# Kernel optimization log

Measured on AMD Instinct MI355X. Metric: run time of the kernel, lower is better.

The kernel has to match this reference:

```python
import jax, jax.numpy as jnp
import numpy as np

H = 1024      # hidden_size
NH = 16       # num_heads
HD = H // NH  # head_dim
BETA = 1.0
STEPS = 2
EPS_NORM = 1e-12  # F.normalize eps
EPS_LN = 1e-5     # LayerNorm eps


def setup_inputs() -> dict:
    key = jax.random.key(0)
    ks = jax.random.split(key, 10)
    s = 1.0 / np.sqrt(H)
    return {
        "hidden_states": jax.random.normal(ks[0], (2, 2048, H), jnp.float32),
        "Wq": jax.random.normal(ks[1], (H, H), jnp.float32) * s,
        "bq": jnp.zeros((H,), jnp.float32),
        "Wk": jax.random.normal(ks[2], (H, H), jnp.float32) * s,
        "bk": jnp.zeros((H,), jnp.float32),
        "Wv": jax.random.normal(ks[3], (H, H), jnp.float32) * s,
        "bv": jnp.zeros((H,), jnp.float32),
        "Wo": jax.random.normal(ks[4], (H, H), jnp.float32) * s,
        "bo": jnp.zeros((H,), jnp.float32),
        "ln_w": jnp.ones((H,), jnp.float32),
        "ln_b": jnp.zeros((H,), jnp.float32),
    }


def _l2norm(x):
    n = jnp.linalg.norm(x, axis=-1, keepdims=True)
    return x / jnp.maximum(n, EPS_NORM)


def reference(hidden_states, Wq, bq, Wk, bk, Wv, bv, Wo, bo, ln_w, ln_b):
    B, S, _ = hidden_states.shape
    residual = hidden_states
    # LayerNorm
    mu = jnp.mean(hidden_states, axis=-1, keepdims=True)
    var = jnp.mean(jnp.square(hidden_states - mu), axis=-1, keepdims=True)
    x = (hidden_states - mu) * jax.lax.rsqrt(var + EPS_LN) * ln_w + ln_b
    # projections -> [B,S,NH,HD]
    q = (x @ Wq + bq).reshape(B, S, NH, HD)
    k = (x @ Wk + bk).reshape(B, S, NH, HD)
    v = (x @ Wv + bv).reshape(B, S, NH, HD)
    # cosine-normalized Hopfield retrieval (normalization only once, before loop)
    q = _l2norm(q)
    k = _l2norm(k)
    state = q
    for _ in range(STEPS):
        sim = jnp.einsum('bqhd,bkhd->bqhk', state, k)
        att = jax.nn.softmax(BETA * sim, axis=-1)
        state = jnp.einsum('bqhk,bkhd->bqhd', att, v)
    o = state.reshape(B, S, H) @ Wo + bo
    return residual + o
```

## Files before the change

kernel.cpp:

```cpp
#include <hip/hip_runtime.h>
#include <hip/hip_bf16.h>
#include <math.h>

#define HDIM 1024
#define NHEADS 16
#define HEADD 64
#define SEQLEN 2048
#define NBATCH 2
#define NROWS (NBATCH*SEQLEN)
#define NBH (NBATCH*NHEADS)
#define LOG2E 1.44269504f
#define NT 32

typedef float f32x4 __attribute__((ext_vector_type(4)));
typedef float f32x16 __attribute__((ext_vector_type(16)));
typedef short short8 __attribute__((ext_vector_type(8)));
typedef unsigned short us4v __attribute__((ext_vector_type(4)));

#define GLOBAL_AS __attribute__((address_space(1)))
#define LDS_AS __attribute__((address_space(3)))

union F4 { float4 v; float f[4]; };
union PW { unsigned int u[4]; short8 s; };

static __device__ __forceinline__ unsigned short f2bf(float x) {
    __hip_bfloat16 h = __float2bfloat16(x);
    return *(unsigned short*)&h;
}

__global__ __launch_bounds__(256) void ln_kernel(
        const float* __restrict__ x, const float* __restrict__ w,
        const float* __restrict__ b, unsigned short* __restrict__ xn) {
    int row = blockIdx.x;
    F4 vv; vv.v = ((const float4*)(x + (size_t)row*HDIM))[threadIdx.x];
    float s  = vv.f[0]+vv.f[1]+vv.f[2]+vv.f[3];
    float ss = vv.f[0]*vv.f[0]+vv.f[1]*vv.f[1]+vv.f[2]*vv.f[2]+vv.f[3]*vv.f[3];
    #pragma unroll
    for (int off = 32; off > 0; off >>= 1) {
        s  += __shfl_xor(s, off);
        ss += __shfl_xor(ss, off);
    }
    __shared__ float red[8];
    int wid = threadIdx.x >> 6;
    if ((threadIdx.x & 63) == 0) { red[wid] = s; red[wid+4] = ss; }
    __syncthreads();
    s  = red[0]+red[1]+red[2]+red[3];
    ss = red[4]+red[5]+red[6]+red[7];
    float mean = s * (1.0f/HDIM);
    float var  = ss * (1.0f/HDIM) - mean*mean;
    float rstd = rsqrtf(var + 1e-5f);
    F4 wv; wv.v = ((const float4*)w)[threadIdx.x];
    F4 bv; bv.v = ((const float4*)b)[threadIdx.x];
    us4v o;
    #pragma unroll
    for (int j = 0; j < 4; ++j)
        o[j] = f2bf((vv.f[j]-mean)*rstd*wv.f[j] + bv.f[j]);
    *(us4v*)(xn + (size_t)row*HDIM + threadIdx.x*4) = o;
}

__global__ __launch_bounds__(256) void wconv_kernel(
        const float* __restrict__ W0, const float* __restrict__ W1,
        const float* __restrict__ W2, const float* __restrict__ W3,
        unsigned short* __restrict__ WtBase) {
    __shared__ unsigned short T[64*72];
    int z = blockIdx.z;
    const float* W = (z == 0) ? W0 : (z == 1) ? W1 : (z == 2) ? W2 : W3;
    unsigned short* Wt = WtBase + (size_t)z*HDIM*HDIM;
    int k0 = blockIdx.x*64, n0 = blockIdx.y*64;
    int t = threadIdx.x;
    #pragma unroll
    for (int it = 0; it < 4; ++it) {
        int r = (t>>4) + it*16;
        int c = (t&15)*4;
        F4 x; x.v = *(const float4*)(W + (size_t)(k0+r)*HDIM + n0 + c);
        #pragma unroll
        for (int j = 0; j < 4; ++j) T[(c+j)*72 + r] = f2bf(x.f[j]);
    }
    __syncthreads();
    #pragma unroll
    for (int it = 0; it < 2; ++it) {
        int n = (t>>3) + it*32;
        int ch = t&7;
        short8 rowv = *(const short8*)(T + n*72 + ch*8);
        *(short8*)(Wt + (size_t)(n0+n)*HDIM + k0 + ch*8) = rowv;
    }
}

__global__ __launch_bounds__(256) void gemm_qkv_kernel(
        const unsigned short* __restrict__ A,
        const unsigned short* __restrict__ WtBase,
        const float* __restrict__ bq, const float* __restrict__ bk,
        const float* __restrict__ bv,
        unsigned short* __restrict__ qb, unsigned short* __restrict__ kb,
        unsigned short* __restrict__ vt) {
    __shared__ unsigned short As[2][128*64];
    __shared__ unsigned short Bs[2][128*64];
    int m0 = blockIdx.x * 128;
    int yy = blockIdx.y;
    int mat = yy >> 3;
    int n0 = (yy & 7) * 128;
    const unsigned short* Wt = WtBase + (size_t)mat*HDIM*HDIM;
    const float* bias = (mat == 0) ? bq : (mat == 1) ? bk : bv;
    int t = threadIdx.x;
    int wid = t >> 6, l = t & 63;
    int wm = wid >> 1, wn = wid & 1;
    int lq = l & 15, g = l >> 4;
    f32x4 acc[4][4];
    #pragma unroll
    for (int mi = 0; mi < 4; ++mi)
        #pragma unroll
        for (int ni = 0; ni < 4; ++ni) acc[mi][ni] = 0.0f;

    auto STAGE = [&](int b, int k0) {
        #pragma unroll
        for (int i = 0; i < 4; ++i) {
            int idx = t + 256*i;
            int r = idx >> 3, ch = idx & 7;
            int gch = ch ^ (r & 7);
            __builtin_amdgcn_global_load_lds(
                (const GLOBAL_AS void*)(A + (size_t)(m0+r)*HDIM + k0 + gch*8),
                (LDS_AS void*)((char*)&As[b][0] + idx*16), 16, 0, 0);
            __builtin_amdgcn_global_load_lds(
                (const GLOBAL_AS void*)(Wt + (size_t)(n0+r)*HDIM + k0 + gch*8),
                (LDS_AS void*)((char*)&Bs[b][0] + idx*16), 16, 0, 0);
        }
    };

    STAGE(0, 0);
    asm volatile("s_waitcnt vmcnt(0)" ::: "memory");
    __builtin_amdgcn_s_barrier();
    asm volatile("" ::: "memory");
    int buf = 0;
    for (int ks = 0; ks < 16; ++ks) {
        if (ks < 15) STAGE(buf^1, (ks+1)*64);
        const char* Ab = (const char*)&As[buf][0];
        const char* Bb = (const char*)&Bs[buf][0];
        #pragma unroll
        for (int kc = 0; kc < 2; ++kc) {
            short8 af[4], bf[4];
            #pragma unroll
            for (int mi = 0; mi < 4; ++mi) {
                int r = wm*64 + mi*16 + lq;
                af[mi] = *(const short8*)(Ab + r*128 + (((kc*4+g) ^ (r&7))<<4));
            }
            #pragma unroll
            for (int ni = 0; ni < 4; ++ni) {
                int r = wn*64 + ni*16 + lq;
                bf[ni] = *(const short8*)(Bb + r*128 + (((kc*4+g) ^ (r&7))<<4));
            }
            #pragma unroll
            for (int mi = 0; mi < 4; ++mi)
                #pragma unroll
                for (int ni = 0; ni < 4; ++ni)
                    acc[mi][ni] = __builtin_amdgcn_mfma_f32_16x16x32_bf16(
                        af[mi], bf[ni], acc[mi][ni], 0, 0, 0);
        }
        asm volatile("s_waitcnt vmcnt(0)" ::: "memory");
        __builtin_amdgcn_s_barrier();
        asm volatile("" ::: "memory");
        buf ^= 1;
    }
    float bvv[4];
    #pragma unroll
    for (int ni = 0; ni < 4; ++ni) bvv[ni] = bias[n0 + wn*64 + ni*16 + lq];
    #pragma unroll
    for (int mi = 0; mi < 4; ++mi)
        #pragma unroll
        for (int ni = 0; ni < 4; ++ni)
            #pragma unroll
            for (int i = 0; i < 4; ++i) acc[mi][ni][i] += bvv[ni];
    int h = (n0 >> 6) + wn;
    if (mat <= 1) {
        unsigned short* outp = (mat == 0) ? qb : kb;
        float oscale = (mat == 0) ? LOG2E : 1.0f;
        #pragma unroll
        for (int mi = 0; mi < 4; ++mi) {
            f32x4 ss = 0.0f;
            #pragma unroll
            for (int ni = 0; ni < 4; ++ni)
                #pragma unroll
                for (int i = 0; i < 4; ++i) ss[i] += acc[mi][ni][i]*acc[mi][ni][i];
            #pragma unroll
            for (int off = 1; off < 16; off <<= 1)
                #pragma unroll
                for (int i = 0; i < 4; ++i) ss[i] += __shfl_xor(ss[i], off);
            #pragma unroll
            for (int i = 0; i < 4; ++i) {
                float sc = oscale / fmaxf(sqrtf(ss[i]), 1e-12f);
                int m = m0 + wm*64 + mi*16 + g*4 + i;
                int bb = m >> 11, sq = m & (SEQLEN-1);
                unsigned short* orow = outp
                    + ((size_t)(bb*NHEADS + h)*SEQLEN + sq)*HEADD;
                #pragma unroll
                for (int ni = 0; ni < 4; ++ni)
                    orow[ni*16 + lq] = f2bf(acc[mi][ni][i] * sc);
            }
        }
    } else {
        #pragma unroll
        for (int mi = 0; mi < 4; ++mi) {
            int m = m0 + wm*64 + mi*16 + g*4;
            int bb = m >> 11, sq = m & (SEQLEN-1);
            #pragma unroll
            for (int ni = 0; ni < 4; ++ni) {
                int d = ni*16 + lq;
                us4v pk;
                #pragma unroll
                for (int i = 0; i < 4; ++i) pk[i] = f2bf(acc[mi][ni][i]);
                *(us4v*)(vt + ((size_t)(bb*NHEADS + h)*HEADD + d)*SEQLEN + sq) = pk;
            }
        }
    }
}

__global__ __launch_bounds__(256) void gemm_o_kernel(
        const unsigned short* __restrict__ A,
        const unsigned short* __restrict__ Wt,
        const float* __restrict__ bias,
        const float* __restrict__ residual,
        float* __restrict__ out) {
    __shared__ unsigned short As[2][128*64];
    __shared__ unsigned short Bs[2][64*64];
    int m0 = blockIdx.x * 128;
    int n0 = blockIdx.y * 64;
    int t = threadIdx.x;
    int wid = t >> 6, l = t & 63;
    int wm = wid >> 1, wn = wid & 1;
    int lq = l & 15, g = l >> 4;
    f32x4 acc[4][2];
    #pragma unroll
    for (int mi = 0; mi < 4; ++mi)
        #pragma unroll
        for (int ni = 0; ni < 2; ++ni) acc[mi][ni] = 0.0f;

    auto STAGE = [&](int b, int k0) {
        #pragma unroll
        for (int i = 0; i < 4; ++i) {
            int idx = t + 256*i;
            int r = idx >> 3, ch = idx & 7;
            int gch = ch ^ (r & 7);
            __builtin_amdgcn_global_load_lds(
                (const GLOBAL_AS void*)(A + (size_t)(m0+r)*HDIM + k0 + gch*8),
                (LDS_AS void*)((char*)&As[b][0] + idx*16), 16, 0, 0);
        }
        #pragma unroll
        for (int i = 0; i < 2; ++i) {
            int idx = t + 256*i;
            int r = idx >> 3, ch = idx & 7;
            int gch = ch ^ (r & 7);
            __builtin_amdgcn_global_load_lds(
                (const GLOBAL_AS void*)(Wt + (size_t)(n0+r)*HDIM + k0 + gch*8),
                (LDS_AS void*)((char*)&Bs[b][0] + idx*16), 16, 0, 0);
        }
    };

    STAGE(0, 0);
    asm volatile("s_waitcnt vmcnt(0)" ::: "memory");
    __builtin_amdgcn_s_barrier();
    asm volatile("" ::: "memory");
    int buf = 0;
    for (int ks = 0; ks < 16; ++ks) {
        if (ks < 15) STAGE(buf^1, (ks+1)*64);
        const char* Ab = (const char*)&As[buf][0];
        const char* Bb = (const char*)&Bs[buf][0];
        #pragma unroll
        for (int kc = 0; kc < 2; ++kc) {
            short8 af[4], bf[2];
            #pragma unroll
            for (int mi = 0; mi < 4; ++mi) {
                int r = wm*64 + mi*16 + lq;
                af[mi] = *(const short8*)(Ab + r*128 + (((kc*4+g) ^ (r&7))<<4));
            }
            #pragma unroll
            for (int ni = 0; ni < 2; ++ni) {
                int r = wn*32 + ni*16 + lq;
                bf[ni] = *(const short8*)(Bb + r*128 + (((kc*4+g) ^ (r&7))<<4));
            }
            #pragma unroll
            for (int mi = 0; mi < 4; ++mi)
                #pragma unroll
                for (int ni = 0; ni < 2; ++ni)
                    acc[mi][ni] = __builtin_amdgcn_mfma_f32_16x16x32_bf16(
                        af[mi], bf[ni], acc[mi][ni], 0, 0, 0);
        }
        asm volatile("s_waitcnt vmcnt(0)" ::: "memory");
        __builtin_amdgcn_s_barrier();
        asm volatile("" ::: "memory");
        buf ^= 1;
    }
    float bvv[2];
    #pragma unroll
    for (int ni = 0; ni < 2; ++ni) bvv[ni] = bias[n0 + wn*32 + ni*16 + lq];
    #pragma unroll
    for (int mi = 0; mi < 4; ++mi)
        #pragma unroll
        for (int i = 0; i < 4; ++i) {
            int m = m0 + wm*64 + mi*16 + g*4 + i;
            float* orow = out + (size_t)m*HDIM;
            const float* rrow = residual + (size_t)m*HDIM;
            #pragma unroll
            for (int ni = 0; ni < 2; ++ni) {
                int n = n0 + wn*32 + ni*16 + lq;
                orow[n] = acc[mi][ni][i] + bvv[ni] + rrow[n];
            }
        }
}

__global__ __launch_bounds__(512, 4) void attn_fused_kernel(
        const unsigned short* __restrict__ qg, const unsigned short* __restrict__ kg,
        const unsigned short* __restrict__ vtg, unsigned short* __restrict__ outp) {
    __shared__ char L[4*16384];
    int b = blockIdx.x;
    int bh = (b & 7)*4 + ((b >> 3) & 3);
    int q0 = (b >> 5) * 128;
    int t = threadIdx.x;
    int wid = t >> 6, l = t & 63;
    int wq = wid >> 1, ks = wid & 1;
    int q = l & 31, hi = l >> 5, r7 = q & 7;
    short8 qf[4];
    {
        const unsigned short* qrow = qg + ((size_t)bh*SEQLEN + q0 + wq*32 + q)*HEADD;
        #pragma unroll
        for (int dc = 0; dc < 4; ++dc) qf[dc] = *(const short8*)(qrow + dc*16 + hi*8);
    }
    int koffK0 = q*128 + (((0 + hi) ^ r7) << 4) + ks*4096;
    int koffK1 = q*128 + (((2 + hi) ^ r7) << 4) + ks*4096;
    int koffK2 = q*128 + (((4 + hi) ^ r7) << 4) + ks*4096;
    int koffK3 = q*128 + (((6 + hi) ^ r7) << 4) + ks*4096;
    int vofA = q*128 + (((4*ks + hi) ^ r7) << 4);
    int vofB = q*128 + (((4*ks + 2 + hi) ^ r7) << 4);

    f32x16 o0 = 0.0f, o1 = 0.0f;
    float ls = 0.0f;
    const unsigned short* Kg = kg + (size_t)bh*SEQLEN*HEADD;
    const unsigned short* Vg = vtg + (size_t)bh*HEADD*SEQLEN;
    unsigned int* slot = (unsigned int*)(L + wq*4096);
    float* slsum = (float*)(L + 16384 + wq*256);

    int sr = t >> 3, sch = t & 7;
    int sgch = sch ^ (sr & 7);
    const unsigned short* Ksrc = Kg + sr*HEADD + sgch*8;
    const unsigned short* Vsrc = Vg + (size_t)sr*SEQLEN + sgch*8;
    auto STAGE = [&](int buf, int kt) {
        __builtin_amdgcn_global_load_lds(
            (const GLOBAL_AS void*)(Ksrc + (size_t)kt*4096),
            (LDS_AS void*)(L + buf*16384 + t*16), 16, 0, 0);
        __builtin_amdgcn_global_load_lds(
            (const GLOBAL_AS void*)(Vsrc + kt*64),
            (LDS_AS void*)(L + buf*16384 + 8192 + t*16), 16, 0, 0);
    };

    auto doPair = [&](const char* A, const char* B) {
        short8 ka0 = *(const short8*)(A + koffK0);
        short8 ka1 = *(const short8*)(A + koffK1);
        short8 ka2 = *(const short8*)(A + koffK2);
        short8 ka3 = *(const short8*)(A + koffK3);
        f32x16 sA = 0.0f;
        sA = __builtin_amdgcn_mfma_f32_32x32x16_bf16(ka0, qf[0], sA, 0, 0, 0);
        sA = __builtin_amdgcn_mfma_f32_32x32x16_bf16(ka1, qf[1], sA, 0, 0, 0);
        sA = __builtin_amdgcn_mfma_f32_32x32x16_bf16(ka2, qf[2], sA, 0, 0, 0);
        sA = __builtin_amdgcn_mfma_f32_32x32x16_bf16(ka3, qf[3], sA, 0, 0, 0);
        __builtin_amdgcn_sched_barrier(0);
        short8 kb0 = *(const short8*)(B + koffK0);
        short8 kb1 = *(const short8*)(B + koffK1);
        short8 kb2 = *(const short8*)(B + koffK2);
        short8 kb3 = *(const short8*)(B + koffK3);
        f32x16 sB = 0.0f;
        sB = __builtin_amdgcn_mfma_f32_32x32x16_bf16(kb0, qf[0], sB, 0, 0, 0);
        sB = __builtin_amdgcn_mfma_f32_32x32x16_bf16(kb1, qf[1], sB, 0, 0, 0);
        sB = __builtin_amdgcn_mfma_f32_32x32x16_bf16(kb2, qf[2], sB, 0, 0, 0);
        sB = __builtin_amdgcn_mfma_f32_32x32x16_bf16(kb3, qf[3], sB, 0, 0, 0);
        __builtin_amdgcn_sched_barrier(0);
        unsigned int wA[8];
        float pA = 0.0f;
        #pragma unroll
        for (int i = 0; i < 8; ++i) {
            float e0 = __builtin_amdgcn_exp2f(sA[2*i]);
            float e1 = __builtin_amdgcn_exp2f(sA[2*i+1]);
            pA += e0 + e1;
            asm("v_cvt_pk_bf16_f32 %0, %1, %2" : "=v"(wA[i]) : "v"(e0), "v"(e1));
        }
        asm volatile("v_permlane32_swap_b32 %0, %1" : "+v"(wA[0]), "+v"(wA[2]));
        asm volatile("v_permlane32_swap_b32 %0, %1" : "+v"(wA[1]), "+v"(wA[3]));
        asm volatile("v_permlane32_swap_b32 %0, %1" : "+v"(wA[4]), "+v"(wA[6]));
        asm volatile("v_permlane32_swap_b32 %0, %1" : "+v"(wA[5]), "+v"(wA[7]));
        __builtin_amdgcn_sched_barrier(0);
        unsigned int wB[8];
        float pB = 0.0f;
        #pragma unroll
        for (int i = 0; i < 8; ++i) {
            float e0 = __builtin_amdgcn_exp2f(sB[2*i]);
            float e1 = __builtin_amdgcn_exp2f(sB[2*i+1]);
            pB += e0 + e1;
            asm("v_cvt_pk_bf16_f32 %0, %1, %2" : "=v"(wB[i]) : "v"(e0), "v"(e1));
        }
        ls += pA + pB;
        asm volatile("v_permlane32_swap_b32 %0, %1" : "+v"(wB[0]), "+v"(wB[2]));
        asm volatile("v_permlane32_swap_b32 %0, %1" : "+v"(wB[1]), "+v"(wB[3]));
        asm volatile("v_permlane32_swap_b32 %0, %1" : "+v"(wB[4]), "+v"(wB[6]));
        asm volatile("v_permlane32_swap_b32 %0, %1" : "+v"(wB[5]), "+v"(wB[7]));
        __builtin_amdgcn_sched_barrier(0);
        {
            PW pa, pb;
            pa.u[0]=wA[0]; pa.u[1]=wA[1]; pa.u[2]=wA[2]; pa.u[3]=wA[3];
            pb.u[0]=wA[4]; pb.u[1]=wA[5]; pb.u[2]=wA[6]; pb.u[3]=wA[7];
            short8 va0 = *(const short8*)(A + 8192 + vofA);
            short8 va1 = *(const short8*)(A + 8192 + vofA + 4096);
            short8 vb0 = *(const short8*)(A + 8192 + vofB);
            short8 vb1 = *(const short8*)(A + 8192 + vofB + 4096);
            __builtin_amdgcn_s_setprio(1);
            o0 = __builtin_amdgcn_mfma_f32_32x32x16_bf16(va0, pa.s, o0, 0, 0, 0);
            o1 = __builtin_amdgcn_mfma_f32_32x32x16_bf16(va1, pa.s, o1, 0, 0, 0);
            o0 = __builtin_amdgcn_mfma_f32_32x32x16_bf16(vb0, pb.s, o0, 0, 0, 0);
            o1 = __builtin_amdgcn_mfma_f32_32x32x16_bf16(vb1, pb.s, o1, 0, 0, 0);
            __builtin_amdgcn_s_setprio(0);
        }
        __builtin_amdgcn_sched_barrier(0);
        {
            PW pa, pb;
            pa.u[0]=wB[0]; pa.u[1]=wB[1]; pa.u[2]=wB[2]; pa.u[3]=wB[3];
            pb.u[0]=wB[4]; pb.u[1]=wB[5]; pb.u[2]=wB[6]; pb.u[3]=wB[7];
            short8 va0 = *(const short8*)(B + 8192 + vofA);
            short8 va1 = *(const short8*)(B + 8192 + vofA + 4096);
            short8 vb0 = *(const short8*)(B + 8192 + vofB);
            short8 vb1 = *(const short8*)(B + 8192 + vofB + 4096);
            __builtin_amdgcn_s_setprio(1);
            o0 = __builtin_amdgcn_mfma_f32_32x32x16_bf16(va0, pa.s, o0, 0, 0, 0);
            o1 = __builtin_amdgcn_mfma_f32_32x32x16_bf16(va1, pa.s, o1, 0, 0, 0);
            o0 = __builtin_amdgcn_mfma_f32_32x32x16_bf16(vb0, pb.s, o0, 0, 0, 0);
            o1 = __builtin_amdgcn_mfma_f32_32x32x16_bf16(vb1, pb.s, o1, 0, 0, 0);
            __builtin_amdgcn_s_setprio(0);
        }
    };

    auto runPass = [&]() {
        #pragma unroll 1
        for (int p = 0; p < NT/2; ++p) {
            int ba = (p & 1) * 2;
            if (p < NT/2 - 1) { STAGE(ba^2, 2*p+2); STAGE((ba^2)+1, 2*p+3); }
            doPair(L + ba*16384, L + (ba+1)*16384);
            asm volatile("s_waitcnt vmcnt(0)" ::: "memory");
            __builtin_amdgcn_s_barrier();
            asm volatile("" ::: "memory");
        }
    };

    STAGE(0, 0); STAGE(1, 1);
    asm volatile("s_waitcnt vmcnt(0)" ::: "memory");
    __builtin_amdgcn_s_barrier();
    asm volatile("" ::: "memory");
    runPass();
    ls += __shfl_xor(ls, 32);
    if (ks == 1) {
        #pragma unroll
        for (int i = 0; i < 8; ++i) {
            unsigned int u;
            asm("v_cvt_pk_bf16_f32 %0, %1, %2" : "=v"(u) : "v"(o0[2*i]), "v"(o0[2*i+1]));
            slot[i*64 + l] = u;
            asm("v_cvt_pk_bf16_f32 %0, %1, %2" : "=v"(u) : "v"(o1[2*i]), "v"(o1[2*i+1]));
            slot[(8+i)*64 + l] = u;
        }
        slsum[l] = ls;
        asm volatile("s_waitcnt lgkmcnt(0)" ::: "memory");
    }
    __builtin_amdgcn_s_barrier();
    asm volatile("" ::: "memory");
    if (ks == 0) {
        #pragma unroll
        for (int i = 0; i < 8; ++i) {
            unsigned int u = slot[i*64 + l];
            o0[2*i]   += __uint_as_float(u << 16);
            o0[2*i+1] += __uint_as_float(u & 0xffff0000u);
            u = slot[(8+i)*64 + l];
            o1[2*i]   += __uint_as_float(u << 16);
            o1[2*i+1] += __uint_as_float(u & 0xffff0000u);
        }
        float osc = LOG2E / (ls + slsum[l]);
        unsigned int w0[8], w1[8];
        #pragma unroll
        for (int i = 0; i < 8; ++i) {
            float a0 = o0[2*i]*osc, a1 = o0[2*i+1]*osc;
            asm("v_cvt_pk_bf16_f32 %0, %1, %2" : "=v"(w0[i]) : "v"(a0), "v"(a1));
            float b0 = o1[2*i]*osc, b1 = o1[2*i+1]*osc;
            asm("v_cvt_pk_bf16_f32 %0, %1, %2" : "=v"(w1[i]) : "v"(b0), "v"(b1));
        }
        asm volatile("v_permlane32_swap_b32 %0, %1" : "+v"(w0[0]), "+v"(w0[2]));
        asm volatile("v_permlane32_swap_b32 %0, %1" : "+v"(w0[1]), "+v"(w0[3]));
        asm volatile("v_permlane32_swap_b32 %0, %1" : "+v"(w0[4]), "+v"(w0[6]));
        asm volatile("v_permlane32_swap_b32 %0, %1" : "+v"(w0[5]), "+v"(w0[7]));
        asm volatile("v_permlane32_swap_b32 %0, %1" : "+v"(w1[0]), "+v"(w1[2]));
        asm volatile("v_permlane32_swap_b32 %0, %1" : "+v"(w1[1]), "+v"(w1[3]));
        asm volatile("v_permlane32_swap_b32 %0, %1" : "+v"(w1[4]), "+v"(w1[6]));
        asm volatile("v_permlane32_swap_b32 %0, %1" : "+v"(w1[5]), "+v"(w1[7]));
        PW pa;
        pa.u[0]=w0[0]; pa.u[1]=w0[1]; pa.u[2]=w0[2]; pa.u[3]=w0[3]; qf[0]=pa.s;
        pa.u[0]=w0[4]; pa.u[1]=w0[5]; pa.u[2]=w0[6]; pa.u[3]=w0[7]; qf[1]=pa.s;
        pa.u[0]=w1[0]; pa.u[1]=w1[1]; pa.u[2]=w1[2]; pa.u[3]=w1[3]; qf[2]=pa.s;
        pa.u[0]=w1[4]; pa.u[1]=w1[5]; pa.u[2]=w1[6]; pa.u[3]=w1[7]; qf[3]=pa.s;
        #pragma unroll
        for (int i = 0; i < 8; ++i) {
            slot[i*64 + l] = w0[i];
            slot[(8+i)*64 + l] = w1[i];
        }
        asm volatile("s_waitcnt lgkmcnt(0)" ::: "memory");
    }
    __builtin_amdgcn_s_barrier();
    asm volatile("" ::: "memory");
    if (ks == 1) {
        PW pa;
        pa.u[0]=slot[0*64+l]; pa.u[1]=slot[1*64+l]; pa.u[2]=slot[2*64+l]; pa.u[3]=slot[3*64+l]; qf[0]=pa.s;
        pa.u[0]=slot[4*64+l]; pa.u[1]=slot[5*64+l]; pa.u[2]=slot[6*64+l]; pa.u[3]=slot[7*64+l]; qf[1]=pa.s;
        pa.u[0]=slot[8*64+l]; pa.u[1]=slot[9*64+l]; pa.u[2]=slot[10*64+l]; pa.u[3]=slot[11*64+l]; qf[2]=pa.s;
        pa.u[0]=slot[12*64+l]; pa.u[1]=slot[13*64+l]; pa.u[2]=slot[14*64+l]; pa.u[3]=slot[15*64+l]; qf[3]=pa.s;
    }
    asm volatile("s_waitcnt lgkmcnt(0)" ::: "memory");
    __builtin_amdgcn_s_barrier();
    asm volatile("" ::: "memory");
    o0 = 0.0f; o1 = 0.0f; ls = 0.0f;
    STAGE(0, 0); STAGE(1, 1);
    asm volatile("s_waitcnt vmcnt(0)" ::: "memory");
    __builtin_amdgcn_s_barrier();
    asm volatile("" ::: "memory");
    runPass();
    ls += __shfl_xor(ls, 32);
    if (ks == 1) {
        #pragma unroll
        for (int i = 0; i < 8; ++i) {
            unsigned int u;
            asm("v_cvt_pk_bf16_f32 %0, %1, %2" : "=v"(u) : "v"(o0[2*i]), "v"(o0[2*i+1]));
            slot[i*64 + l] = u;
            asm("v_cvt_pk_bf16_f32 %0, %1, %2" : "=v"(u) : "v"(o1[2*i]), "v"(o1[2*i+1]));
            slot[(8+i)*64 + l] = u;
        }
        slsum[l] = ls;
        asm volatile("s_waitcnt lgkmcnt(0)" ::: "memory");
    }
    __builtin_amdgcn_s_barrier();
    asm volatile("" ::: "memory");
    if (ks == 0) {
        #pragma unroll
        for (int i = 0; i < 8; ++i) {
            unsigned int u = slot[i*64 + l];
            o0[2*i]   += __uint_as_float(u << 16);
            o0[2*i+1] += __uint_as_float(u & 0xffff0000u);
            u = slot[(8+i)*64 + l];
            o1[2*i]   += __uint_as_float(u << 16);
            o1[2*i+1] += __uint_as_float(u & 0xffff0000u);
        }
        float osc = 1.0f / (ls + slsum[l]);
        int bb = bh >> 4, hh = bh & 15;
        unsigned short* orow = outp + ((size_t)bb*SEQLEN + q0 + wq*32 + q)*HDIM + hh*HEADD;
        const int dtab[8] = {0,2,8,10,16,18,24,26};
        #pragma unroll
        for (int i = 0; i < 8; ++i) {
            int d = dtab[i] + 4*hi;
            unsigned int wv;
            float a0 = o0[2*i]*osc, a1 = o0[2*i+1]*osc;
            asm("v_cvt_pk_bf16_f32 %0, %1, %2" : "=v"(wv) : "v"(a0), "v"(a1));
            *(unsigned int*)(orow + d) = wv;
            float c0 = o1[2*i]*osc, c1 = o1[2*i+1]*osc;
            asm("v_cvt_pk_bf16_f32 %0, %1, %2" : "=v"(wv) : "v"(c0), "v"(c1));
            *(unsigned int*)(orow + 32 + d) = wv;
        }
    }
}

extern "C" void kernel_launch(void* const* d_in, const int* in_sizes, int n_in,
                              void* d_out, int out_size, void* d_ws, size_t ws_size,
                              hipStream_t stream) {
    const float* hs = (const float*)d_in[0];
    const float* Wq = (const float*)d_in[1];
    const float* bq = (const float*)d_in[2];
    const float* Wk = (const float*)d_in[3];
    const float* bk = (const float*)d_in[4];
    const float* Wv = (const float*)d_in[5];
    const float* bv = (const float*)d_in[6];
    const float* Wo = (const float*)d_in[7];
    const float* bo = (const float*)d_in[8];
    const float* lw = (const float*)d_in[9];
    const float* lb = (const float*)d_in[10];
    unsigned short* ws16 = (unsigned short*)d_ws;
    const size_t NE = (size_t)NROWS * HDIM;
    const size_t WE = (size_t)HDIM * HDIM;
    unsigned short* xn  = ws16;
    unsigned short* Wtq = xn + NE;
    unsigned short* Wto = Wtq + 3*WE;
    unsigned short* qb  = Wtq + 4*WE;
    unsigned short* kb  = qb + NE;
    unsigned short* vt  = kb + NE;
    unsigned short* s2  = vt + NE;

    ln_kernel<<<NROWS, 256, 0, stream>>>(hs, lw, lb, xn);
    wconv_kernel<<<dim3(HDIM/64, HDIM/64, 4), 256, 0, stream>>>(Wq, Wk, Wv, Wo, Wtq);
    gemm_qkv_kernel<<<dim3(NROWS/128, 24), 256, 0, stream>>>(xn, Wtq, bq, bk, bv, qb, kb, vt);
    attn_fused_kernel<<<NBH*16, 512, 0, stream>>>(qb, kb, vt, s2);
    gemm_o_kernel<<<dim3(NROWS/128, HDIM/64), 256, 0, stream>>>(s2, Wto, bo, hs, (float*)d_out);
}
```

Baseline: 163.2 us.

## Double queries per attention block to reuse each K/V tile twice

Each wave now handles two 32-row query groups (A and B) against every staged K/V tile, so a block covers 256 queries and the grid halves. K and V fragments loaded from LDS are shared by both groups, which halves global K/V traffic and LDS reads per query. In exchange, register pressure doubles for accumulators and Q fragments, occupancy drops (launch bounds go from 4 to 2), and there are half as many blocks (256) to spread across the CUs.

```diff
diff --git a/kernel.cpp b/kernel.cpp
--- a/kernel.cpp
+++ b/kernel.cpp
@@ -306,22 +306,26 @@
         }
 }
 
-__global__ __launch_bounds__(512, 4) void attn_fused_kernel(
+__global__ __launch_bounds__(512, 2) void attn_fused_kernel(
         const unsigned short* __restrict__ qg, const unsigned short* __restrict__ kg,
         const unsigned short* __restrict__ vtg, unsigned short* __restrict__ outp) {
     __shared__ char L[4*16384];
     int b = blockIdx.x;
     int bh = (b & 7)*4 + ((b >> 3) & 3);
-    int q0 = (b >> 5) * 128;
+    int q0 = (b >> 5) * 256;
     int t = threadIdx.x;
     int wid = t >> 6, l = t & 63;
     int wq = wid >> 1, ks = wid & 1;
     int q = l & 31, hi = l >> 5, r7 = q & 7;
-    short8 qf[4];
+    short8 qfA[4], qfB[4];
     {
-        const unsigned short* qrow = qg + ((size_t)bh*SEQLEN + q0 + wq*32 + q)*HEADD;
-        #pragma unroll
-        for (int dc = 0; dc < 4; ++dc) qf[dc] = *(const short8*)(qrow + dc*16 + hi*8);
+        const unsigned short* qrowA = qg + ((size_t)bh*SEQLEN + q0 + wq*64 + q)*HEADD;
+        const unsigned short* qrowB = qrowA + 32*HEADD;
+        #pragma unroll
+        for (int dc = 0; dc < 4; ++dc) {
+            qfA[dc] = *(const short8*)(qrowA + dc*16 + hi*8);
+            qfB[dc] = *(const short8*)(qrowB + dc*16 + hi*8);
+        }
     }
     int koffK0 = q*128 + (((0 + hi) ^ r7) << 4) + ks*4096;
     int koffK1 = q*128 + (((2 + hi) ^ r7) << 4) + ks*4096;
@@ -330,12 +334,14 @@
     int vofA = q*128 + (((4*ks + hi) ^ r7) << 4);
     int vofB = q*128 + (((4*ks + 2 + hi) ^ r7) << 4);
 
-    f32x16 o0 = 0.0f, o1 = 0.0f;
-    float ls = 0.0f;
+    f32x16 oA0 = 0.0f, oA1 = 0.0f, oB0 = 0.0f, oB1 = 0.0f;
+    float lsA = 0.0f, lsB = 0.0f;
     const unsigned short* Kg = kg + (size_t)bh*SEQLEN*HEADD;
     const unsigned short* Vg = vtg + (size_t)bh*HEADD*SEQLEN;
-    unsigned int* slot = (unsigned int*)(L + wq*4096);
-    float* slsum = (float*)(L + 16384 + wq*256);
+    unsigned int* slotA = (unsigned int*)(L + wq*4096);
+    unsigned int* slotB = (unsigned int*)(L + 16384 + wq*4096);
+    float* slsA = (float*)(L + 32768 + wq*512);
+    float* slsB = slsA + 64;
 
     int sr = t >> 3, sch = t & 7;
     int sgch = sch ^ (sr & 7);
@@ -350,26 +356,22 @@
             (LDS_AS void*)(L + buf*16384 + 8192 + t*16), 16, 0, 0);
     };
 
-    auto doPair = [&](const char* A, const char* B) {
-        short8 ka0 = *(const short8*)(A + koffK0);
-        short8 ka1 = *(const short8*)(A + koffK1);
-        short8 ka2 = *(const short8*)(A + koffK2);
-        short8 ka3 = *(const short8*)(A + koffK3);
+    auto doTile = [&](const char* T) {
+        short8 k0 = *(const short8*)(T + koffK0);
+        short8 k1 = *(const short8*)(T + koffK1);
+        short8 k2 = *(const short8*)(T + koffK2);
+        short8 k3 = *(const short8*)(T + koffK3);
         f32x16 sA = 0.0f;
-        sA = __builtin_amdgcn_mfma_f32_32x32x16_bf16(ka0, qf[0], sA, 0, 0, 0);
-        sA = __builtin_amdgcn_mfma_f32_32x32x16_bf16(ka1, qf[1], sA, 0, 0, 0);
-        sA = __builtin_amdgcn_mfma_f32_32x32x16_bf16(ka2, qf[2], sA, 0, 0, 0);
-        sA = __builtin_amdgcn_mfma_f32_32x32x16_bf16(ka3, qf[3], sA, 0, 0, 0);
+        sA = __builtin_amdgcn_mfma_f32_32x32x16_bf16(k0, qfA[0], sA, 0, 0, 0);
+        sA = __builtin_amdgcn_mfma_f32_32x32x16_bf16(k1, qfA[1], sA, 0, 0, 0);
+        sA = __builtin_amdgcn_mfma_f32_32x32x16_bf16(k2, qfA[2], sA, 0, 0, 0);
+        sA = __builtin_amdgcn_mfma_f32_32x32x16_bf16(k3, qfA[3], sA, 0, 0, 0);
         __builtin_amdgcn_sched_barrier(0);
-        short8 kb0 = *(const short8*)(B + koffK0);
-        short8 kb1 = *(const short8*)(B + koffK1);
-        short8 kb2 = *(const short8*)(B + koffK2);
-        short8 kb3 = *(const short8*)(B + koffK3);
         f32x16 sB = 0.0f;
-        sB = __builtin_amdgcn_mfma_f32_32x32x16_bf16(kb0, qf[0], sB, 0, 0, 0);
-        sB = __builtin_amdgcn_mfma_f32_32x32x16_bf16(kb1, qf[1], sB, 0, 0, 0);
-        sB = __builtin_amdgcn_mfma_f32_32x32x16_bf16(kb2, qf[2], sB, 0, 0, 0);
-        sB = __builtin_amdgcn_mfma_f32_32x32x16_bf16(kb3, qf[3], sB, 0, 0, 0);
+        sB = __builtin_amdgcn_mfma_f32_32x32x16_bf16(k0, qfB[0], sB, 0, 0, 0);
+        sB = __builtin_amdgcn_mfma_f32_32x32x16_bf16(k1, qfB[1], sB, 0, 0, 0);
+        sB = __builtin_amdgcn_mfma_f32_32x32x16_bf16(k2, qfB[2], sB, 0, 0, 0);
+        sB = __builtin_amdgcn_mfma_f32_32x32x16_bf16(k3, qfB[3], sB, 0, 0, 0);
         __builtin_amdgcn_sched_barrier(0);
         unsigned int wA[8];
         float pA = 0.0f;
@@ -380,10 +382,16 @@
             pA += e0 + e1;
             asm("v_cvt_pk_bf16_f32 %0, %1, %2" : "=v"(wA[i]) : "v"(e0), "v"(e1));
         }
-        asm volatile("v_permlane32_swap_b32 %0, %1" : "+v"(wA[0]), "+v"(wA[2]));
-        asm volatile("v_permlane32_swap_b32 %0, %1" : "+v"(wA[1]), "+v"(wA[3]));
-        asm volatile("v_permlane32_swap_b32 %0, %1" : "+v"(wA[4]), "+v"(wA[6]));
-        asm volatile("v_permlane32_swap_b32 %0, %1" : "+v"(wA[5]), "+v"(wA[7]));
+        lsA += pA;
+        asm("v_permlane32_swap_b32 %0, %1" : "+v"(wA[0]), "+v"(wA[2]));
+        asm("v_permlane32_swap_b32 %0, %1" : "+v"(wA[1]), "+v"(wA[3]));
+        asm("v_permlane32_swap_b32 %0, %1" : "+v"(wA[4]), "+v"(wA[6]));
+        asm("v_permlane32_swap_b32 %0, %1" : "+v"(wA[5]), "+v"(wA[7]));
+        __builtin_amdgcn_sched_barrier(0);
+        short8 va0 = *(const short8*)(T + 8192 + vofA);
+        short8 va1 = *(const short8*)(T + 8192 + vofA + 4096);
+        short8 vb0 = *(const short8*)(T + 8192 + vofB);
+        short8 vb1 = *(const short8*)(T + 8192 + vofB + 4096);
         __builtin_amdgcn_sched_barrier(0);
         unsigned int wB[8];
         float pB = 0.0f;
@@ -394,25 +402,21 @@
             pB += e0 + e1;
             asm("v_cvt_pk_bf16_f32 %0, %1, %2" : "=v"(wB[i]) : "v"(e0), "v"(e1));
         }
-        ls += pA + pB;
-        asm volatile("v_permlane32_swap_b32 %0, %1" : "+v"(wB[0]), "+v"(wB[2]));
-        asm volatile("v_permlane32_swap_b32 %0, %1" : "+v"(wB[1]), "+v"(wB[3]));
-        asm volatile("v_permlane32_swap_b32 %0, %1" : "+v"(wB[4]), "+v"(wB[6]));
-        asm volatile("v_permlane32_swap_b32 %0, %1" : "+v"(wB[5]), "+v"(wB[7]));
+        lsB += pB;
+        asm("v_permlane32_swap_b32 %0, %1" : "+v"(wB[0]), "+v"(wB[2]));
+        asm("v_permlane32_swap_b32 %0, %1" : "+v"(wB[1]), "+v"(wB[3]));
+        asm("v_permlane32_swap_b32 %0, %1" : "+v"(wB[4]), "+v"(wB[6]));
+        asm("v_permlane32_swap_b32 %0, %1" : "+v"(wB[5]), "+v"(wB[7]));
         __builtin_amdgcn_sched_barrier(0);
         {
             PW pa, pb;
             pa.u[0]=wA[0]; pa.u[1]=wA[1]; pa.u[2]=wA[2]; pa.u[3]=wA[3];
             pb.u[0]=wA[4]; pb.u[1]=wA[5]; pb.u[2]=wA[6]; pb.u[3]=wA[7];
-            short8 va0 = *(const short8*)(A + 8192 + vofA);
-            short8 va1 = *(const short8*)(A + 8192 + vofA + 4096);
-            short8 vb0 = *(const short8*)(A + 8192 + vofB);
-            short8 vb1 = *(const short8*)(A + 8192 + vofB + 4096);
             __builtin_amdgcn_s_setprio(1);
-            o0 = __builtin_amdgcn_mfma_f32_32x32x16_bf16(va0, pa.s, o0, 0, 0, 0);
-            o1 = __builtin_amdgcn_mfma_f32_32x32x16_bf16(va1, pa.s, o1, 0, 0, 0);
-            o0 = __builtin_amdgcn_mfma_f32_32x32x16_bf16(vb0, pb.s, o0, 0, 0, 0);
-            o1 = __builtin_amdgcn_mfma_f32_32x32x16_bf16(vb1, pb.s, o1, 0, 0, 0);
+            oA0 = __builtin_amdgcn_mfma_f32_32x32x16_bf16(va0, pa.s, oA0, 0, 0, 0);
+            oA1 = __builtin_amdgcn_mfma_f32_32x32x16_bf16(va1, pa.s, oA1, 0, 0, 0);
+            oA0 = __builtin_amdgcn_mfma_f32_32x32x16_bf16(vb0, pb.s, oA0, 0, 0, 0);
+            oA1 = __builtin_amdgcn_mfma_f32_32x32x16_bf16(vb1, pb.s, oA1, 0, 0, 0);
             __builtin_amdgcn_s_setprio(0);
         }
         __builtin_amdgcn_sched_barrier(0);
@@ -420,15 +424,11 @@
             PW pa, pb;
             pa.u[0]=wB[0]; pa.u[1]=wB[1]; pa.u[2]=wB[2]; pa.u[3]=wB[3];
             pb.u[0]=wB[4]; pb.u[1]=wB[5]; pb.u[2]=wB[6]; pb.u[3]=wB[7];
-            short8 va0 = *(const short8*)(B + 8192 + vofA);
-            short8 va1 = *(const short8*)(B + 8192 + vofA + 4096);
-            short8 vb0 = *(const short8*)(B + 8192 + vofB);
-            short8 vb1 = *(const short8*)(B + 8192 + vofB + 4096);
             __builtin_amdgcn_s_setprio(1);
-            o0 = __builtin_amdgcn_mfma_f32_32x32x16_bf16(va0, pa.s, o0, 0, 0, 0);
-            o1 = __builtin_amdgcn_mfma_f32_32x32x16_bf16(va1, pa.s, o1, 0, 0, 0);
-            o0 = __builtin_amdgcn_mfma_f32_32x32x16_bf16(vb0, pb.s, o0, 0, 0, 0);
-            o1 = __builtin_amdgcn_mfma_f32_32x32x16_bf16(vb1, pb.s, o1, 0, 0, 0);
+            oB0 = __builtin_amdgcn_mfma_f32_32x32x16_bf16(va0, pa.s, oB0, 0, 0, 0);
+            oB1 = __builtin_amdgcn_mfma_f32_32x32x16_bf16(va1, pa.s, oB1, 0, 0, 0);
+            oB0 = __builtin_amdgcn_mfma_f32_32x32x16_bf16(vb0, pb.s, oB0, 0, 0, 0);
+            oB1 = __builtin_amdgcn_mfma_f32_32x32x16_bf16(vb1, pb.s, oB1, 0, 0, 0);
             __builtin_amdgcn_s_setprio(0);
         }
     };
@@ -438,7 +438,8 @@
         for (int p = 0; p < NT/2; ++p) {
             int ba = (p & 1) * 2;
             if (p < NT/2 - 1) { STAGE(ba^2, 2*p+2); STAGE((ba^2)+1, 2*p+3); }
-            doPair(L + ba*16384, L + (ba+1)*16384);
+            doTile(L + ba*16384);
+            doTile(L + (ba+1)*16384);
             asm volatile("s_waitcnt vmcnt(0)" ::: "memory");
             __builtin_amdgcn_s_barrier();
             asm volatile("" ::: "memory");
@@ -450,17 +451,23 @@
     __builtin_amdgcn_s_barrier();
     asm volatile("" ::: "memory");
     runPass();
-    ls += __shfl_xor(ls, 32);
+    lsA += __shfl_xor(lsA, 32);
+    lsB += __shfl_xor(lsB, 32);
     if (ks == 1) {
         #pragma unroll
         for (int i = 0; i < 8; ++i) {
             unsigned int u;
-            asm("v_cvt_pk_bf16_f32 %0, %1, %2" : "=v"(u) : "v"(o0[2*i]), "v"(o0[2*i+1]));
-            slot[i*64 + l] = u;
-            asm("v_cvt_pk_bf16_f32 %0, %1, %2" : "=v"(u) : "v"(o1[2*i]), "v"(o1[2*i+1]));
-            slot[(8+i)*64 + l] = u;
-        }
-        slsum[l] = ls;
+            asm("v_cvt_pk_bf16_f32 %0, %1, %2" : "=v"(u) : "v"(oA0[2*i]), "v"(oA0[2*i+1]));
+            slotA[i*64 + l] = u;
+            asm("v_cvt_pk_bf16_f32 %0, %1, %2" : "=v"(u) : "v"(oA1[2*i]), "v"(oA1[2*i+1]));
+            slotA[(8+i)*64 + l] = u;
+            asm("v_cvt_pk_bf16_f32 %0, %1, %2" : "=v"(u) : "v"(oB0[2*i]), "v"(oB0[2*i+1]));
+            slotB[i*64 + l] = u;
+            asm("v_cvt_pk_bf16_f32 %0, %1, %2" : "=v"(u) : "v"(oB1[2*i]), "v"(oB1[2*i+1]));
+            slotB[(8+i)*64 + l] = u;
+        }
+        slsA[l] = lsA;
+        slsB[l] = lsB;
         asm volatile("s_waitcnt lgkmcnt(0)" ::: "memory");
     }
     __builtin_amdgcn_s_barrier();
@@ -468,21 +475,32 @@
     if (ks == 0) {
         #pragma unroll
         for (int i = 0; i < 8; ++i) {
-            unsigned int u = slot[i*64 + l];
-            o0[2*i]   += __uint_as_float(u << 16);
-            o0[2*i+1] += __uint_as_float(u & 0xffff0000u);
-            u = slot[(8+i)*64 + l];
-            o1[2*i]   += __uint_as_float(u << 16);
-            o1[2*i+1] += __uint_as_float(u & 0xffff0000u);
-        }
-        float osc = LOG2E / (ls + slsum[l]);
-        unsigned int w0[8], w1[8];
-        #pragma unroll
-        for (int i = 0; i < 8; ++i) {
-            float a0 = o0[2*i]*osc, a1 = o0[2*i+1]*osc;
+            unsigned int u = slotA[i*64 + l];
+            oA0[2*i]   += __uint_as_float(u << 16);
+            oA0[2*i+1] += __uint_as_float(u & 0xffff0000u);
+            u = slotA[(8+i)*64 + l];
+            oA1[2*i]   += __uint_as_float(u << 16);
+            oA1[2*i+1] += __uint_as_float(u & 0xffff0000u);
+            u = slotB[i*64 + l];
+            oB0[2*i]   += __uint_as_float(u << 16);
+            oB0[2*i+1] += __uint_as_float(u & 0xffff0000u);
+            u = slotB[(8+i)*64 + l];
+            oB1[2*i]   += __uint_as_float(u << 16);
+            oB1[2*i+1] += __uint_as_float(u & 0xffff0000u);
+        }
+        float oscA = LOG2E / (lsA + slsA[l]);
+        float oscB = LOG2E / (lsB + slsB[l]);
+        unsigned int w0[8], w1[8], w2[8], w3[8];
+        #pragma unroll
+        for (int i = 0; i < 8; ++i) {
+            float a0 = oA0[2*i]*oscA, a1 = oA0[2*i+1]*oscA;
             asm("v_cvt_pk_bf16_f32 %0, %1, %2" : "=v"(w0[i]) : "v"(a0), "v"(a1));
-            float b0 = o1[2*i]*osc, b1 = o1[2*i+1]*osc;
+            float b0 = oA1[2*i]*oscA, b1 = oA1[2*i+1]*oscA;
             asm("v_cvt_pk_bf16_f32 %0, %1, %2" : "=v"(w1[i]) : "v"(b0), "v"(b1));
+            float c0 = oB0[2*i]*oscB, c1 = oB0[2*i+1]*oscB;
+            asm("v_cvt_pk_bf16_f32 %0, %1, %2" : "=v"(w2[i]) : "v"(c0), "v"(c1));
+            float d0 = oB1[2*i]*oscB, d1 = oB1[2*i+1]*oscB;
+            asm("v_cvt_pk_bf16_f32 %0, %1, %2" : "=v"(w3[i]) : "v"(d0), "v"(d1));
         }
         asm volatile("v_permlane32_swap_b32 %0, %1" : "+v"(w0[0]), "+v"(w0[2]));
         asm volatile("v_permlane32_swap_b32 %0, %1" : "+v"(w0[1]), "+v"(w0[3]));
@@ -492,15 +510,29 @@
         asm volatile("v_permlane32_swap_b32 %0, %1" : "+v"(w1[1]), "+v"(w1[3]));
         asm volatile("v_permlane32_swap_b32 %0, %1" : "+v"(w1[4]), "+v"(w1[6]));
         asm volatile("v_permlane32_swap_b32 %0, %1" : "+v"(w1[5]), "+v"(w1[7]));
+        asm volatile("v_permlane32_swap_b32 %0, %1" : "+v"(w2[0]), "+v"(w2[2]));
+        asm volatile("v_permlane32_swap_b32 %0, %1" : "+v"(w2[1]), "+v"(w2[3]));
+        asm volatile("v_permlane32_swap_b32 %0, %1" : "+v"(w2[4]), "+v"(w2[6]));
+        asm volatile("v_permlane32_swap_b32 %0, %1" : "+v"(w2[5]), "+v"(w2[7]));
+        asm volatile("v_permlane32_swap_b32 %0, %1" : "+v"(w3[0]), "+v"(w3[2]));
+        asm volatile("v_permlane32_swap_b32 %0, %1" : "+v"(w3[1]), "+v"(w3[3]));
+        asm volatile("v_permlane32_swap_b32 %0, %1" : "+v"(w3[4]), "+v"(w3[6]));
+        asm volatile("v_permlane32_swap_b32 %0, %1" : "+v"(w3[5]), "+v"(w3[7]));
         PW pa;
-        pa.u[0]=w0[0]; pa.u[1]=w0[1]; pa.u[2]=w0[2]; pa.u[3]=w0[3]; qf[0]=pa.s;
-        pa.u[0]=w0[4]; pa.u[1]=w0[5]; pa.u[2]=w0[6]; pa.u[3]=w0[7]; qf[1]=pa.s;
-        pa.u[0]=w1[0]; pa.u[1]=w1[1]; pa.u[2]=w1[2]; pa.u[3]=w1[3]; qf[2]=pa.s;
-        pa.u[0]=w1[4]; pa.u[1]=w1[5]; pa.u[2]=w1[6]; pa.u[3]=w1[7]; qf[3]=pa.s;
-        #pragma unroll
-        for (int i = 0; i < 8; ++i) {
-            slot[i*64 + l] = w0[i];
-            slot[(8+i)*64 + l] = w1[i];
+        pa.u[0]=w0[0]; pa.u[1]=w0[1]; pa.u[2]=w0[2]; pa.u[3]=w0[3]; qfA[0]=pa.s;
+        pa.u[0]=w0[4]; pa.u[1]=w0[5]; pa.u[2]=w0[6]; pa.u[3]=w0[7]; qfA[1]=pa.s;
+        pa.u[0]=w1[0]; pa.u[1]=w1[1]; pa.u[2]=w1[2]; pa.u[3]=w1[3]; qfA[2]=pa.s;
+        pa.u[0]=w1[4]; pa.u[1]=w1[5]; pa.u[2]=w1[6]; pa.u[3]=w1[7]; qfA[3]=pa.s;
+        pa.u[0]=w2[0]; pa.u[1]=w2[1]; pa.u[2]=w2[2]; pa.u[3]=w2[3]; qfB[0]=pa.s;
+        pa.u[0]=w2[4]; pa.u[1]=w2[5]; pa.u[2]=w2[6]; pa.u[3]=w2[7]; qfB[1]=pa.s;
+        pa.u[0]=w3[0]; pa.u[1]=w3[1]; pa.u[2]=w3[2]; pa.u[3]=w3[3]; qfB[2]=pa.s;
+        pa.u[0]=w3[4]; pa.u[1]=w3[5]; pa.u[2]=w3[6]; pa.u[3]=w3[7]; qfB[3]=pa.s;
+        #pragma unroll
+        for (int i = 0; i < 8; ++i) {
+            slotA[i*64 + l] = w0[i];
+            slotA[(8+i)*64 + l] = w1[i];
+            slotB[i*64 + l] = w2[i];
+            slotB[(8+i)*64 + l] = w3[i];
         }
         asm volatile("s_waitcnt lgkmcnt(0)" ::: "memory");
     }
@@ -508,31 +540,41 @@
     asm volatile("" ::: "memory");
     if (ks == 1) {
         PW pa;
-        pa.u[0]=slot[0*64+l]; pa.u[1]=slot[1*64+l]; pa.u[2]=slot[2*64+l]; pa.u[3]=slot[3*64+l]; qf[0]=pa.s;
-        pa.u[0]=slot[4*64+l]; pa.u[1]=slot[5*64+l]; pa.u[2]=slot[6*64+l]; pa.u[3]=slot[7*64+l]; qf[1]=pa.s;
-        pa.u[0]=slot[8*64+l]; pa.u[1]=slot[9*64+l]; pa.u[2]=slot[10*64+l]; pa.u[3]=slot[11*64+l]; qf[2]=pa.s;
-        pa.u[0]=slot[12*64+l]; pa.u[1]=slot[13*64+l]; pa.u[2]=slot[14*64+l]; pa.u[3]=slot[15*64+l]; qf[3]=pa.s;
+        pa.u[0]=slotA[0*64+l]; pa.u[1]=slotA[1*64+l]; pa.u[2]=slotA[2*64+l]; pa.u[3]=slotA[3*64+l]; qfA[0]=pa.s;
+        pa.u[0]=slotA[4*64+l]; pa.u[1]=slotA[5*64+l]; pa.u[2]=slotA[6*64+l]; pa.u[3]=slotA[7*64+l]; qfA[1]=pa.s;
+        pa.u[0]=slotA[8*64+l]; pa.u[1]=slotA[9*64+l]; pa.u[2]=slotA[10*64+l]; pa.u[3]=slotA[11*64+l]; qfA[2]=pa.s;
+        pa.u[0]=slotA[12*64+l]; pa.u[1]=slotA[13*64+l]; pa.u[2]=slotA[14*64+l]; pa.u[3]=slotA[15*64+l]; qfA[3]=pa.s;
+        pa.u[0]=slotB[0*64+l]; pa.u[1]=slotB[1*64+l]; pa.u[2]=slotB[2*64+l]; pa.u[3]=slotB[3*64+l]; qfB[0]=pa.s;
+        pa.u[0]=slotB[4*64+l]; pa.u[1]=slotB[5*64+l]; pa.u[2]=slotB[6*64+l]; pa.u[3]=slotB[7*64+l]; qfB[1]=pa.s;
+        pa.u[0]=slotB[8*64+l]; pa.u[1]=slotB[9*64+l]; pa.u[2]=slotB[10*64+l]; pa.u[3]=slotB[11*64+l]; qfB[2]=pa.s;
+        pa.u[0]=slotB[12*64+l]; pa.u[1]=slotB[13*64+l]; pa.u[2]=slotB[14*64+l]; pa.u[3]=slotB[15*64+l]; qfB[3]=pa.s;
     }
     asm volatile("s_waitcnt lgkmcnt(0)" ::: "memory");
     __builtin_amdgcn_s_barrier();
     asm volatile("" ::: "memory");
-    o0 = 0.0f; o1 = 0.0f; ls = 0.0f;
+    oA0 = 0.0f; oA1 = 0.0f; oB0 = 0.0f; oB1 = 0.0f; lsA = 0.0f; lsB = 0.0f;
     STAGE(0, 0); STAGE(1, 1);
     asm volatile("s_waitcnt vmcnt(0)" ::: "memory");
     __builtin_amdgcn_s_barrier();
     asm volatile("" ::: "memory");
     runPass();
-    ls += __shfl_xor(ls, 32);
+    lsA += __shfl_xor(lsA, 32);
+    lsB += __shfl_xor(lsB, 32);
     if (ks == 1) {
         #pragma unroll
         for (int i = 0; i < 8; ++i) {
             unsigned int u;
-            asm("v_cvt_pk_bf16_f32 %0, %1, %2" : "=v"(u) : "v"(o0[2*i]), "v"(o0[2*i+1]));
-            slot[i*64 + l] = u;
-            asm("v_cvt_pk_bf16_f32 %0, %1, %2" : "=v"(u) : "v"(o1[2*i]), "v"(o1[2*i+1]));
-            slot[(8+i)*64 + l] = u;
-        }
-        slsum[l] = ls;
+            asm("v_cvt_pk_bf16_f32 %0, %1, %2" : "=v"(u) : "v"(oA0[2*i]), "v"(oA0[2*i+1]));
+            slotA[i*64 + l] = u;
+            asm("v_cvt_pk_bf16_f32 %0, %1, %2" : "=v"(u) : "v"(oA1[2*i]), "v"(oA1[2*i+1]));
+            slotA[(8+i)*64 + l] = u;
+            asm("v_cvt_pk_bf16_f32 %0, %1, %2" : "=v"(u) : "v"(oB0[2*i]), "v"(oB0[2*i+1]));
+            slotB[i*64 + l] = u;
+            asm("v_cvt_pk_bf16_f32 %0, %1, %2" : "=v"(u) : "v"(oB1[2*i]), "v"(oB1[2*i+1]));
+            slotB[(8+i)*64 + l] = u;
+        }
+        slsA[l] = lsA;
+        slsB[l] = lsB;
         asm volatile("s_waitcnt lgkmcnt(0)" ::: "memory");
     }
     __builtin_amdgcn_s_barrier();
@@ -540,27 +582,42 @@
     if (ks == 0) {
         #pragma unroll
         for (int i = 0; i < 8; ++i) {
-            unsigned int u = slot[i*64 + l];
-            o0[2*i]   += __uint_as_float(u << 16);
-            o0[2*i+1] += __uint_as_float(u & 0xffff0000u);
-            u = slot[(8+i)*64 + l];
-            o1[2*i]   += __uint_as_float(u << 16);
-            o1[2*i+1] += __uint_as_float(u & 0xffff0000u);
-        }
-        float osc = 1.0f / (ls + slsum[l]);
+            unsigned int u = slotA[i*64 + l];
+            oA0[2*i]   += __uint_as_float(u << 16);
+            oA0[2*i+1] += __uint_as_float(u & 0xffff0000u);
+            u = slotA[(8+i)*64 + l];
+            oA1[2*i]   += __uint_as_float(u << 16);
+            oA1[2*i+1] += __uint_as_float(u & 0xffff0000u);
+            u = slotB[i*64 + l];
+            oB0[2*i]   += __uint_as_float(u << 16);
+            oB0[2*i+1] += __uint_as_float(u & 0xffff0000u);
+            u = slotB[(8+i)*64 + l];
+            oB1[2*i]   += __uint_as_float(u << 16);
+            oB1[2*i+1] += __uint_as_float(u & 0xffff0000u);
+        }
+        float oscA = 1.0f / (lsA + slsA[l]);
+        float oscB = 1.0f / (lsB + slsB[l]);
         int bb = bh >> 4, hh = bh & 15;
-        unsigned short* orow = outp + ((size_t)bb*SEQLEN + q0 + wq*32 + q)*HDIM + hh*HEADD;
+        int rowA = q0 + wq*64 + q;
+        unsigned short* orowA = outp + ((size_t)bb*SEQLEN + rowA)*HDIM + hh*HEADD;
+        unsigned short* orowB = orowA + 32*HDIM;
         const int dtab[8] = {0,2,8,10,16,18,24,26};
         #pragma unroll
         for (int i = 0; i < 8; ++i) {
             int d = dtab[i] + 4*hi;
             unsigned int wv;
-            float a0 = o0[2*i]*osc, a1 = o0[2*i+1]*osc;
+            float a0 = oA0[2*i]*oscA, a1 = oA0[2*i+1]*oscA;
             asm("v_cvt_pk_bf16_f32 %0, %1, %2" : "=v"(wv) : "v"(a0), "v"(a1));
-            *(unsigned int*)(orow + d) = wv;
-            float c0 = o1[2*i]*osc, c1 = o1[2*i+1]*osc;
+            *(unsigned int*)(orowA + d) = wv;
+            float b0 = oA1[2*i]*oscA, b1 = oA1[2*i+1]*oscA;
+            asm("v_cvt_pk_bf16_f32 %0, %1, %2" : "=v"(wv) : "v"(b0), "v"(b1));
+            *(unsigned int*)(orowA + 32 + d) = wv;
+            float c0 = oB0[2*i]*oscB, c1 = oB0[2*i+1]*oscB;
             asm("v_cvt_pk_bf16_f32 %0, %1, %2" : "=v"(wv) : "v"(c0), "v"(c1));
-            *(unsigned int*)(orow + 32 + d) = wv;
+            *(unsigned int*)(orowB + d) = wv;
+            float d0 = oB1[2*i]*oscB, d1 = oB1[2*i+1]*oscB;
+            asm("v_cvt_pk_bf16_f32 %0, %1, %2" : "=v"(wv) : "v"(d0), "v"(d1));
+            *(unsigned int*)(orowB + 32 + d) = wv;
         }
     }
 }
@@ -593,6 +650,6 @@
     ln_kernel<<<NROWS, 256, 0, stream>>>(hs, lw, lb, xn);
     wconv_kernel<<<dim3(HDIM/64, HDIM/64, 4), 256, 0, stream>>>(Wq, Wk, Wv, Wo, Wtq);
     gemm_qkv_kernel<<<dim3(NROWS/128, 24), 256, 0, stream>>>(xn, Wtq, bq, bk, bv, qb, kb, vt);
-    attn_fused_kernel<<<NBH*16, 512, 0, stream>>>(qb, kb, vt, s2);
+    attn_fused_kernel<<<NBH*8, 512, 0, stream>>>(qb, kb, vt, s2);
     gemm_o_kernel<<<dim3(NROWS/128, HDIM/64), 256, 0, stream>>>(s2, Wto, bo, hs, (float*)d_out);
 }
```

After: 154.9 us. -5.1%, faster.
